# Kernel tuning notes

Measured on AMD Instinct MI355X. Metric: run time of the kernel, lower is better.

Reference implementation:

```python
import jax, jax.numpy as jnp
import numpy as np

WORLD_SIZE = 8
M_LOCAL = 1024  # max_M // world_size
K = 4096
N = 4096


def setup_inputs() -> dict:
    key = jax.random.key(0)
    k1, k2 = jax.random.split(key)
    # per-rank input shards; all-gather concatenates them along M
    input_shards = jax.random.normal(k1, (WORLD_SIZE, M_LOCAL, K), dtype=jnp.float32)
    # weight stored [N, K] (transed_weight=False path: weight.shape[1] == K)
    weight = jax.random.normal(k2, (N, K), dtype=jnp.float32) * 0.02
    return {"input_shards": input_shards, "weight": weight, "transed_weight": 0}


def reference(input_shards, weight, transed_weight):
    # All-gather across ranks along M: concat shards -> [max_M, K]
    gathered = input_shards.reshape(-1, input_shards.shape[-1])
    # GEMM: out[m, n] = sum_k gathered[m, k] * W[k, n]
    w_kn = weight if transed_weight else weight.T  # -> [K, N]
    return jnp.einsum("mk,kn->mn", gathered, w_kn)
```

## Files before the change

### kernel.cpp

```cpp
#include <hip/hip_runtime.h>
#include <stdint.h>

#define K_DIM 4096
#define N_DIM 4096
#define BM 256
#define BN 256
#define NTILES (K_DIM / 64)
#define NIT (NTILES / 2)

typedef short short8 __attribute__((ext_vector_type(8)));
typedef float f32x4 __attribute__((ext_vector_type(4)));
typedef unsigned short ushort_t;
typedef unsigned short ushort8 __attribute__((ext_vector_type(8)));

__device__ __forceinline__ ushort_t f2bf(float f) {
    uint32_t u = __float_as_uint(f);
    u += 0x7FFFu + ((u >> 16) & 1u);
    return (ushort_t)(u >> 16);
}

__global__ void cast_to_bf16_2(const float* __restrict__ a, const float* __restrict__ w,
                               ushort_t* __restrict__ out_a, ushort_t* __restrict__ out_w,
                               int n8a, int n8w) {
    int i = blockIdx.x * blockDim.x + threadIdx.x;
    const float* in;
    ushort_t* out;
    int j;
    if (i < n8a) { in = a; out = out_a; j = i; }
    else if (i < n8a + n8w) { in = w; out = out_w; j = i - n8a; }
    else return;
    const float4* p = (const float4*)in + (size_t)j * 2;
    float4 v0 = p[0];
    float4 v1 = p[1];
    ushort8 r;
    r[0] = f2bf(v0.x); r[1] = f2bf(v0.y); r[2] = f2bf(v0.z); r[3] = f2bf(v0.w);
    r[4] = f2bf(v1.x); r[5] = f2bf(v1.y); r[6] = f2bf(v1.z); r[7] = f2bf(v1.w);
    *((ushort8*)out + j) = r;
}

__device__ __forceinline__ void wgbar() {
    asm volatile("" ::: "memory");
    __builtin_amdgcn_s_barrier();
    asm volatile("" ::: "memory");
}


#define LDS_A(b, kk) (sA + ((b) * 2 + (kk)) * 8192)
#define LDS_B(b, kk) (sB + ((b) * 2 + (kk)) * 8192)

#define LOAD_AF(af, b, kk, mih) { _Pragma("unroll") for (int t = 0; t < 4; ++t) { \
    int row = wm + (mih) * 64 + t * 16 + row16;                                   \
    af[t] = *(const short8*)(LDS_A(b, kk) + row * 32 + ksw * 8); } }

#define LOAD_BF(bfr, b, kk) { _Pragma("unroll") for (int t = 0; t < 4; ++t) {     \
    int row = wn + t * 16 + row16;                                                \
    bfr[t] = *(const short8*)(LDS_B(b, kk) + row * 32 + ksw * 8); } }

#define MFMA16(mih, af, bfr) { __builtin_amdgcn_s_setprio(1);                     \
    _Pragma("unroll") for (int t = 0; t < 4; ++t)                                 \
    _Pragma("unroll") for (int n = 0; n < 4; ++n)                                 \
        acc[(mih) * 4 + t][n] = __builtin_amdgcn_mfma_f32_16x16x32_bf16(          \
            af[t], bfr[n], acc[(mih) * 4 + t][n], 0, 0, 0);                       \
    __builtin_amdgcn_s_setprio(0); }

#define LGKM0() asm volatile("s_waitcnt lgkmcnt(0)")
#define VMCNT4() asm volatile("s_waitcnt vmcnt(4)" ::: "memory")

__global__ __launch_bounds__(512, 2) void gemm_bf16_8ph(
    const ushort_t* __restrict__ A,
    const ushort_t* __restrict__ B,
    float* __restrict__ C)
{
    __shared__ ushort_t sA[2 * 2 * 8192];
    __shared__ ushort_t sB[2 * 2 * 8192];

    const int pid0 = blockIdx.x;
    const int pid  = (pid0 & 7) * (int)(gridDim.x >> 3) + (pid0 >> 3);
    const int pid_n = pid & 15;
    const int pid_m = pid >> 4;
    const int tile_m = pid_m * BM;
    const int tile_n = pid_n * BN;

    const int lane  = threadIdx.x & 63;
    const int wave  = threadIdx.x >> 6;
    const int wm    = (wave >> 2) * 128;
    const int wn    = (wave & 3) * 64;
    const int row16 = lane & 15;
    const int quad  = lane >> 4;
    const int ksw   = quad ^ ((row16 >> 1) & 3);

    int cb[2];
    size_t goff[2];
    #pragma unroll
    for (int j = 0; j < 2; ++j) {
        cb[j] = wave * 64 + j * 512;
        int c = cb[j] + lane;
        int r = c >> 2;
        int q = (c & 3) ^ ((r >> 1) & 3);
        goff[j] = (size_t)r * K_DIM + q * 8;
    }
    const ushort_t* Abase = A + (size_t)tile_m * K_DIM;
    const ushort_t* Bbase = B + (size_t)tile_n * K_DIM;

    auto STAGE = [&](const ushort_t* gbase, ushort_t* lds, int k0) {
        #pragma unroll
        for (int j = 0; j < 2; ++j) {
            const ushort_t* gp = gbase + goff[j] + k0;
            __builtin_amdgcn_global_load_lds(
                (const __attribute__((address_space(1))) void*)gp,
                (__attribute__((address_space(3))) void*)(lds + cb[j] * 8), 16, 0, 0);
        }
    };

    f32x4 acc[8][4] = {};

    STAGE(Abase, LDS_A(0, 0), 0);
    STAGE(Bbase, LDS_B(0, 0), 0);
    STAGE(Abase, LDS_A(0, 1), 32);
    STAGE(Bbase, LDS_B(0, 1), 32);
    STAGE(Abase, LDS_A(1, 0), 64);
    STAGE(Bbase, LDS_B(1, 0), 64);
    VMCNT4();
    wgbar();

    short8 af[4], bfr[4];

    #pragma unroll 1
    for (int i = 0; i < NIT; ++i) {
        const int k1 = (2 * i + 1) * 64;
        int t2 = 2 * i + 2; if (t2 > NTILES - 1) t2 = NTILES - 1;
        int t3 = 2 * i + 3; if (t3 > NTILES - 1) t3 = NTILES - 1;
        const int k2 = t2 * 64, k3 = t3 * 64;

        LOAD_AF(af, 0, 0, 0); LOAD_BF(bfr, 0, 0);
        STAGE(Abase, LDS_A(1, 1), k1 + 32);
        wgbar(); LGKM0();
        MFMA16(0, af, bfr);
        wgbar();

        LOAD_AF(af, 0, 0, 1);
        STAGE(Bbase, LDS_B(1, 1), k1 + 32);
        wgbar(); LGKM0();
        MFMA16(1, af, bfr);
        wgbar();

        LOAD_AF(af, 0, 1, 0); LOAD_BF(bfr, 0, 1);
        STAGE(Abase, LDS_A(0, 0), k2);
        wgbar(); LGKM0();
        MFMA16(0, af, bfr);
        wgbar();

        LOAD_AF(af, 0, 1, 1);
        STAGE(Bbase, LDS_B(0, 0), k2);
        VMCNT4();
        wgbar(); LGKM0();
        MFMA16(1, af, bfr);
        wgbar();

        LOAD_AF(af, 1, 0, 0); LOAD_BF(bfr, 1, 0);
        STAGE(Abase, LDS_A(0, 1), k2 + 32);
        wgbar(); LGKM0();
        MFMA16(0, af, bfr);
        wgbar();

        LOAD_AF(af, 1, 0, 1);
        STAGE(Bbase, LDS_B(0, 1), k2 + 32);
        wgbar(); LGKM0();
        MFMA16(1, af, bfr);
        wgbar();

        LOAD_AF(af, 1, 1, 0); LOAD_BF(bfr, 1, 1);
        STAGE(Abase, LDS_A(1, 0), k3);
        wgbar(); LGKM0();
        MFMA16(0, af, bfr);
        wgbar();

        LOAD_AF(af, 1, 1, 1);
        STAGE(Bbase, LDS_B(1, 0), k3);
        VMCNT4();
        wgbar(); LGKM0();
        MFMA16(1, af, bfr);
        wgbar();
    }

    #pragma unroll
    for (int mi = 0; mi < 8; ++mi) {
        #pragma unroll
        for (int r = 0; r < 4; ++r) {
            int m = tile_m + wm + mi * 16 + quad * 4 + r;
            float* crow = C + (size_t)m * N_DIM + tile_n + wn;
            #pragma unroll
            for (int n = 0; n < 4; ++n)
                crow[n * 16 + row16] = acc[mi][n][r];
        }
    }
}

__global__ void gemm_naive_f32(const float* __restrict__ A, const float* __restrict__ W,
                               float* __restrict__ C, int m_tot) {
    int n = blockIdx.x * blockDim.x + threadIdx.x;
    int m = blockIdx.y;
    if (n >= N_DIM || m >= m_tot) return;
    const float* a = A + (size_t)m * K_DIM;
    const float* w = W + (size_t)n * K_DIM;
    float s = 0.f;
    for (int k = 0; k < K_DIM; ++k) s += a[k] * w[k];
    C[(size_t)m * N_DIM + n] = s;
}

extern "C" void kernel_launch(void* const* d_in, const int* in_sizes, int n_in,
                              void* d_out, int out_size, void* d_ws, size_t ws_size,
                              hipStream_t stream) {
    const float* a_f32 = (const float*)d_in[0];
    const float* w_f32 = (const float*)d_in[1];
    float* out = (float*)d_out;

    const size_t a_elems = (size_t)in_sizes[0];
    const size_t w_elems = (size_t)in_sizes[1];
    const int m_tot = (int)(a_elems / K_DIM);

    const size_t need = (a_elems + w_elems) * sizeof(ushort_t);
    if (ws_size >= need && (m_tot % BM) == 0 && w_elems == (size_t)N_DIM * K_DIM) {
        ushort_t* a_bf = (ushort_t*)d_ws;
        ushort_t* w_bf = a_bf + a_elems;

        int n8a = (int)(a_elems / 8);
        int n8w = (int)(w_elems / 8);
        int n8 = n8a + n8w;
        cast_to_bf16_2<<<(n8 + 255) / 256, 256, 0, stream>>>(a_f32, w_f32, a_bf, w_bf, n8a, n8w);

        int nblocks = (N_DIM / BN) * (m_tot / BM);
        gemm_bf16_8ph<<<nblocks, 512, 0, stream>>>(a_bf, w_bf, out);
    } else {
        dim3 grid(N_DIM / 256, m_tot);
        gemm_naive_f32<<<grid, 256, 0, stream>>>(a_f32, w_f32, out, m_tot);
    }
}
```

Before: 499.8 us.

## Fuse fp32-to-bf16 conversion into GEMM staging, drop separate cast kernel

Removes the standalone cast kernel and its bf16 workspace round-trip. The GEMM now loads fp32 tiles into registers, converts them with v_cvt_pk_bf16_f32, and writes the swizzled bf16 values to LDS, in place of direct global_load_lds DMA. This cuts a full extra read and write of A and W in HBM plus one kernel launch. In exchange, the GEMM reads twice as many bytes per tile from global memory and spends VGPRs and VALU time on staging and conversion. The register-held prefetch also relies on an implicit vmcnt wait before each conversion.

New measurement: 551.4 us. +10.3%, slower.

```diff
diff --git a/kernel.cpp b/kernel.cpp
--- a/kernel.cpp
+++ b/kernel.cpp
@@ -10,33 +10,9 @@
 
 typedef short short8 __attribute__((ext_vector_type(8)));
 typedef float f32x4 __attribute__((ext_vector_type(4)));
+typedef float f32x4v __attribute__((ext_vector_type(4)));
+typedef uint32_t u32x4 __attribute__((ext_vector_type(4)));
 typedef unsigned short ushort_t;
-typedef unsigned short ushort8 __attribute__((ext_vector_type(8)));
-
-__device__ __forceinline__ ushort_t f2bf(float f) {
-    uint32_t u = __float_as_uint(f);
-    u += 0x7FFFu + ((u >> 16) & 1u);
-    return (ushort_t)(u >> 16);
-}
-
-__global__ void cast_to_bf16_2(const float* __restrict__ a, const float* __restrict__ w,
-                               ushort_t* __restrict__ out_a, ushort_t* __restrict__ out_w,
-                               int n8a, int n8w) {
-    int i = blockIdx.x * blockDim.x + threadIdx.x;
-    const float* in;
-    ushort_t* out;
-    int j;
-    if (i < n8a) { in = a; out = out_a; j = i; }
-    else if (i < n8a + n8w) { in = w; out = out_w; j = i - n8a; }
-    else return;
-    const float4* p = (const float4*)in + (size_t)j * 2;
-    float4 v0 = p[0];
-    float4 v1 = p[1];
-    ushort8 r;
-    r[0] = f2bf(v0.x); r[1] = f2bf(v0.y); r[2] = f2bf(v0.z); r[3] = f2bf(v0.w);
-    r[4] = f2bf(v1.x); r[5] = f2bf(v1.y); r[6] = f2bf(v1.z); r[7] = f2bf(v1.w);
-    *((ushort8*)out + j) = r;
-}
 
 __device__ __forceinline__ void wgbar() {
     asm volatile("" ::: "memory");
@@ -64,11 +40,28 @@
     __builtin_amdgcn_s_setprio(0); }
 
 #define LGKM0() asm volatile("s_waitcnt lgkmcnt(0)")
-#define VMCNT4() asm volatile("s_waitcnt vmcnt(4)" ::: "memory")
 
-__global__ __launch_bounds__(512, 2) void gemm_bf16_8ph(
-    const ushort_t* __restrict__ A,
-    const ushort_t* __restrict__ B,
+#define ISSUE(base, k) {                                                          \
+    const float* _p0 = (base) + off0 + (k);                                       \
+    const float* _p1 = (base) + off1 + (k);                                       \
+    S0a = *(const f32x4v*)_p0; S0b = *(const f32x4v*)(_p0 + 4);                   \
+    S1a = *(const f32x4v*)_p1; S1b = *(const f32x4v*)(_p1 + 4); }
+
+#define CVTW(ldsp) { uint32_t w0, w1, w2, w3, w4, w5, w6, w7;                     \
+    asm("v_cvt_pk_bf16_f32 %0, %1, %2" : "=v"(w0) : "v"(S0a[0]), "v"(S0a[1]));    \
+    asm("v_cvt_pk_bf16_f32 %0, %1, %2" : "=v"(w1) : "v"(S0a[2]), "v"(S0a[3]));    \
+    asm("v_cvt_pk_bf16_f32 %0, %1, %2" : "=v"(w2) : "v"(S0b[0]), "v"(S0b[1]));    \
+    asm("v_cvt_pk_bf16_f32 %0, %1, %2" : "=v"(w3) : "v"(S0b[2]), "v"(S0b[3]));    \
+    asm("v_cvt_pk_bf16_f32 %0, %1, %2" : "=v"(w4) : "v"(S1a[0]), "v"(S1a[1]));    \
+    asm("v_cvt_pk_bf16_f32 %0, %1, %2" : "=v"(w5) : "v"(S1a[2]), "v"(S1a[3]));    \
+    asm("v_cvt_pk_bf16_f32 %0, %1, %2" : "=v"(w6) : "v"(S1b[0]), "v"(S1b[1]));    \
+    asm("v_cvt_pk_bf16_f32 %0, %1, %2" : "=v"(w7) : "v"(S1b[2]), "v"(S1b[3]));    \
+    *(u32x4*)((ldsp) + dst0 * 8) = (u32x4){w0, w1, w2, w3};                       \
+    *(u32x4*)((ldsp) + dst1 * 8) = (u32x4){w4, w5, w6, w7}; }
+
+__global__ __launch_bounds__(512, 2) void gemm_fused_f32_8ph(
+    const float* __restrict__ A,
+    const float* __restrict__ B,
     float* __restrict__ C)
 {
     __shared__ ushort_t sA[2 * 2 * 8192];
@@ -89,98 +82,71 @@
     const int quad  = lane >> 4;
     const int ksw   = quad ^ ((row16 >> 1) & 3);
 
-    int cb[2];
-    size_t goff[2];
-    #pragma unroll
-    for (int j = 0; j < 2; ++j) {
-        cb[j] = wave * 64 + j * 512;
-        int c = cb[j] + lane;
-        int r = c >> 2;
-        int q = (c & 3) ^ ((r >> 1) & 3);
-        goff[j] = (size_t)r * K_DIM + q * 8;
-    }
-    const ushort_t* Abase = A + (size_t)tile_m * K_DIM;
-    const ushort_t* Bbase = B + (size_t)tile_n * K_DIM;
+    const int c0 = wave * 64 + lane;
+    const int c1 = c0 + 512;
+    const int r0 = c0 >> 2, g0 = c0 & 3;
+    const int r1 = c1 >> 2, g1 = c1 & 3;
+    const int off0 = r0 * K_DIM + g0 * 8;
+    const int off1 = r1 * K_DIM + g1 * 8;
+    const int dst0 = r0 * 4 + (g0 ^ ((r0 >> 1) & 3));
+    const int dst1 = r1 * 4 + (g1 ^ ((r1 >> 1) & 3));
 
-    auto STAGE = [&](const ushort_t* gbase, ushort_t* lds, int k0) {
-        #pragma unroll
-        for (int j = 0; j < 2; ++j) {
-            const ushort_t* gp = gbase + goff[j] + k0;
-            __builtin_amdgcn_global_load_lds(
-                (const __attribute__((address_space(1))) void*)gp,
-                (__attribute__((address_space(3))) void*)(lds + cb[j] * 8), 16, 0, 0);
-        }
-    };
+    const float* Af = A + (size_t)tile_m * K_DIM;
+    const float* Bf = B + (size_t)tile_n * K_DIM;
 
+    f32x4v S0a, S0b, S1a, S1b;
     f32x4 acc[8][4] = {};
 
-    STAGE(Abase, LDS_A(0, 0), 0);
-    STAGE(Bbase, LDS_B(0, 0), 0);
-    STAGE(Abase, LDS_A(0, 1), 32);
-    STAGE(Bbase, LDS_B(0, 1), 32);
-    STAGE(Abase, LDS_A(1, 0), 64);
-    STAGE(Bbase, LDS_B(1, 0), 64);
-    VMCNT4();
+    ISSUE(Af, 0);   CVTW(LDS_A(0, 0));
+    ISSUE(Bf, 0);   CVTW(LDS_B(0, 0));
+    ISSUE(Af, 32);  CVTW(LDS_A(0, 1));
+    ISSUE(Bf, 32);  CVTW(LDS_B(0, 1));
+    ISSUE(Af, 64);  CVTW(LDS_A(1, 0));
+    ISSUE(Bf, 64);  CVTW(LDS_B(1, 0));
+    ISSUE(Af, 96);
+    LGKM0();
     wgbar();
 
     short8 af[4], bfr[4];
 
     #pragma unroll 1
     for (int i = 0; i < NIT; ++i) {
-        const int k1 = (2 * i + 1) * 64;
+        const int t1k = (2 * i + 1) * 64;
         int t2 = 2 * i + 2; if (t2 > NTILES - 1) t2 = NTILES - 1;
         int t3 = 2 * i + 3; if (t3 > NTILES - 1) t3 = NTILES - 1;
         const int k2 = t2 * 64, k3 = t3 * 64;
 
         LOAD_AF(af, 0, 0, 0); LOAD_BF(bfr, 0, 0);
-        STAGE(Abase, LDS_A(1, 1), k1 + 32);
-        wgbar(); LGKM0();
-        MFMA16(0, af, bfr);
-        wgbar();
+        CVTW(LDS_A(1, 1)); ISSUE(Bf, t1k + 32);
+        wgbar(); LGKM0(); MFMA16(0, af, bfr); wgbar();
 
         LOAD_AF(af, 0, 0, 1);
-        STAGE(Bbase, LDS_B(1, 1), k1 + 32);
-        wgbar(); LGKM0();
-        MFMA16(1, af, bfr);
-        wgbar();
+        CVTW(LDS_B(1, 1)); ISSUE(Af, k2);
+        wgbar(); LGKM0(); MFMA16(1, af, bfr); wgbar();
 
         LOAD_AF(af, 0, 1, 0); LOAD_BF(bfr, 0, 1);
-        STAGE(Abase, LDS_A(0, 0), k2);
-        wgbar(); LGKM0();
-        MFMA16(0, af, bfr);
-        wgbar();
+        CVTW(LDS_A(0, 0)); ISSUE(Bf, k2);
+        wgbar(); LGKM0(); MFMA16(0, af, bfr); wgbar();
 
         LOAD_AF(af, 0, 1, 1);
-        STAGE(Bbase, LDS_B(0, 0), k2);
-        VMCNT4();
-        wgbar(); LGKM0();
-        MFMA16(1, af, bfr);
-        wgbar();
+        CVTW(LDS_B(0, 0)); ISSUE(Af, k2 + 32);
+        wgbar(); LGKM0(); MFMA16(1, af, bfr); wgbar();
 
         LOAD_AF(af, 1, 0, 0); LOAD_BF(bfr, 1, 0);
-        STAGE(Abase, LDS_A(0, 1), k2 + 32);
-        wgbar(); LGKM0();
-        MFMA16(0, af, bfr);
-        wgbar();
+        CVTW(LDS_A(0, 1)); ISSUE(Bf, k2 + 32);
+        wgbar(); LGKM0(); MFMA16(0, af, bfr); wgbar();
 
         LOAD_AF(af, 1, 0, 1);
-        STAGE(Bbase, LDS_B(0, 1), k2 + 32);
-        wgbar(); LGKM0();
-        MFMA16(1, af, bfr);
-        wgbar();
+        CVTW(LDS_B(0, 1)); ISSUE(Af, k3);
+        wgbar(); LGKM0(); MFMA16(1, af, bfr); wgbar();
 
         LOAD_AF(af, 1, 1, 0); LOAD_BF(bfr, 1, 1);
-        STAGE(Abase, LDS_A(1, 0), k3);
-        wgbar(); LGKM0();
-        MFMA16(0, af, bfr);
-        wgbar();
+        CVTW(LDS_A(1, 0)); ISSUE(Bf, k3);
+        wgbar(); LGKM0(); MFMA16(0, af, bfr); wgbar();
 
         LOAD_AF(af, 1, 1, 1);
-        STAGE(Bbase, LDS_B(1, 0), k3);
-        VMCNT4();
-        wgbar(); LGKM0();
-        MFMA16(1, af, bfr);
-        wgbar();
+        CVTW(LDS_B(1, 0)); ISSUE(Af, k3 + 32);
+        wgbar(); LGKM0(); MFMA16(1, af, bfr); wgbar();
     }
 
     #pragma unroll
@@ -219,18 +185,10 @@
     const size_t w_elems = (size_t)in_sizes[1];
     const int m_tot = (int)(a_elems / K_DIM);
 
-    const size_t need = (a_elems + w_elems) * sizeof(ushort_t);
-    if (ws_size >= need && (m_tot % BM) == 0 && w_elems == (size_t)N_DIM * K_DIM) {
-        ushort_t* a_bf = (ushort_t*)d_ws;
-        ushort_t* w_bf = a_bf + a_elems;
-
-        int n8a = (int)(a_elems / 8);
-        int n8w = (int)(w_elems / 8);
-        int n8 = n8a + n8w;
-        cast_to_bf16_2<<<(n8 + 255) / 256, 256, 0, stream>>>(a_f32, w_f32, a_bf, w_bf, n8a, n8w);
-
+    if ((m_tot % BM) == 0 && w_elems == (size_t)N_DIM * K_DIM &&
+        a_elems == (size_t)m_tot * K_DIM) {
         int nblocks = (N_DIM / BN) * (m_tot / BM);
-        gemm_bf16_8ph<<<nblocks, 512, 0, stream>>>(a_bf, w_bf, out);
+        gemm_fused_f32_8ph<<<nblocks, 512, 0, stream>>>(a_f32, w_f32, out);
     } else {
         dim3 grid(N_DIM / 256, m_tot);
         gemm_naive_f32<<<grid, 256, 0, stream>>>(a_f32, w_f32, out, m_tot);
```
